# Kernel tuning notes

Hardware: AMD Instinct MI355X
Metric: run time of the kernel (lower is better)

## Reference

```python
import jax, jax.numpy as jnp
import numpy as np

E2M1_GRID = jnp.array([0.0, 0.5, 1.0, 1.5, 2.0, 3.0, 4.0, 6.0], dtype=jnp.float32)
E2M1_MIDS = (E2M1_GRID[1:] + E2M1_GRID[:-1]) / 2.0
FP4_MAX = 6.0
FP8_E4M3_MAX = 448.0


def nvfp4_quant_dequant(w):
    # Emulates tetrajetv2.quant_fp4_dequant_trans_fused: two-level scaling
    # (fp32 outer scale per 128 inputs, fp8-e4m3 inner scale per 16 inputs),
    # values rounded to the signed E2M1 grid, then dequantized.
    O, I = w.shape
    w16 = w.reshape(O, I // 128, 8, 16)
    amax128 = jnp.max(jnp.abs(w16), axis=(-2, -1))          # [O, I/128]
    outer = amax128 / (FP4_MAX * FP8_E4M3_MAX)
    outer = jnp.where(outer > 0, outer, 1.0)
    amax16 = jnp.max(jnp.abs(w16), axis=-1)                  # [O, I/128, 8]
    inner = amax16 / FP4_MAX / outer[..., None]
    inner = inner.astype(jnp.float8_e4m3fn).astype(jnp.float32)  # fp8 round
    scale = outer[..., None] * inner                          # [O, I/128, 8]
    safe = jnp.where(scale > 0, scale, 1.0)[..., None]
    code = w16 / safe
    a = jnp.abs(code)
    idx = jnp.searchsorted(E2M1_MIDS, a)                      # nearest grid pt
    q = E2M1_GRID[idx] * jnp.sign(code)
    return (q * scale[..., None]).reshape(O, I)


def setup_inputs() -> dict:
    key = jax.random.key(0)
    k0, k1, k2 = jax.random.split(key, 3)
    B, S, H = 2, 2048, 2048
    hidden_states = jax.random.normal(k0, (B, S, H), dtype=jnp.float32)
    # raw weights ~ N(0, 0.023) as in FP4Linear init, then fake-quantized
    w_qkv = jax.random.normal(k1, (3 * H, H), dtype=jnp.float32) * 0.023
    w_o = jax.random.normal(k2, (H, H), dtype=jnp.float32) * 0.023
    w_qkv = nvfp4_quant_dequant(w_qkv)
    w_o = nvfp4_quant_dequant(w_o)
    return {"hidden_states": hidden_states, "w_qkv": w_qkv, "w_o": w_o}


def reference(hidden_states, w_qkv, w_o):
    B, S, H = hidden_states.shape
    num_heads = 16
    head_dim = H // num_heads
    qkv = jnp.einsum('bsh,oh->bso', hidden_states, w_qkv)      # [B,S,3H]
    qkv = qkv.reshape(B, S, 3, num_heads, head_dim)
    qkv = jnp.transpose(qkv, (2, 0, 3, 1, 4))                  # [3,B,nh,S,hd]
    q, k, v = qkv[0], qkv[1], qkv[2]
    scale = 1.0 / jnp.sqrt(jnp.float32(head_dim))
    scores = jnp.einsum('bhqd,bhkd->bhqk', q, k) * scale
    causal = jnp.tril(jnp.ones((S, S), dtype=bool))
    scores = jnp.where(causal, scores, jnp.finfo(scores.dtype).min)
    probs = jax.nn.softmax(scores, axis=-1)
    attn = jnp.einsum('bhqk,bhkd->bhqd', probs, v)             # [B,nh,S,hd]
    attn = jnp.transpose(attn, (0, 2, 1, 3)).reshape(B, S, H)
    return jnp.einsum('bsh,oh->bso', attn, w_o)
```

## Files before the change

### kernel.cpp

```cpp
#include <hip/hip_runtime.h>
#include <hip/hip_bf16.h>
#include <stdint.h>

typedef __bf16 bf16x8 __attribute__((ext_vector_type(8)));
typedef float f32x4 __attribute__((ext_vector_type(4)));

#define AS1 __attribute__((address_space(1)))
#define AS3 __attribute__((address_space(3)))

#define PBAR() do { __builtin_amdgcn_sched_barrier(0); asm volatile("s_barrier" ::: "memory"); __builtin_amdgcn_sched_barrier(0); } while (0)
#define LGK0() do { asm volatile("s_waitcnt lgkmcnt(0)" ::: "memory"); __builtin_amdgcn_sched_barrier(0); } while (0)
#define VMCNT(n) do { asm volatile("s_waitcnt vmcnt(" #n ")" ::: "memory"); __builtin_amdgcn_sched_barrier(0); } while (0)

__device__ __forceinline__ unsigned short f2bf(float x) {
    union { float f; uint32_t u; } v; v.f = x;
    uint32_t r = v.u + 0x7fffu + ((v.u >> 16) & 1u);
    return (unsigned short)(r >> 16);
}

__global__ void k_f2bf3(const float* __restrict__ a, unsigned short* __restrict__ oa, int na4,
                        const float* __restrict__ b, unsigned short* __restrict__ ob, int nb4,
                        const float* __restrict__ c, unsigned short* __restrict__ oc, int nc4) {
    int i = blockIdx.x * blockDim.x + threadIdx.x;
    const float* src; unsigned short* dst; int j;
    if (i < na4)            { src = a; dst = oa; j = i; }
    else if (i < na4 + nb4) { src = b; dst = ob; j = i - na4; }
    else if (i < na4 + nb4 + nc4) { src = c; dst = oc; j = i - na4 - nb4; }
    else return;
    float4 v = reinterpret_cast<const float4*>(src)[j];
    ushort4 o;
    o.x = f2bf(v.x); o.y = f2bf(v.y); o.z = f2bf(v.z); o.w = f2bf(v.w);
    reinterpret_cast<ushort4*>(dst)[j] = o;
}

template <typename TOUT>
__global__ __launch_bounds__(512, 2) void k_gemm128x256(
    const unsigned short* __restrict__ A,
    const unsigned short* __restrict__ B,
    TOUT* __restrict__ C, int M, int N, int K, int ngrid)
{
    __shared__ __align__(16) unsigned short Albuf[3][4096];
    __shared__ __align__(16) unsigned short Blbuf[3][8192];
    const int tid = threadIdx.x, lane = tid & 63, wv = tid >> 6;
    const int wr = wv >> 2, wc = wv & 3;
    const int fl = lane & 15, fg = lane >> 4;
    const int cpx = ngrid >> 3;
    const int sw = ((int)blockIdx.x & 7) * cpx + ((int)blockIdx.x >> 3);
    const int bm = sw & 31, bn = sw >> 5;
    const int nK = K >> 5;

    const unsigned short* Ag = A + (size_t)bm * 128 * K;
    const unsigned short* Bg = B + (size_t)bn * 256 * K;

    auto stageA = [&](int buf, int t) {
        const int r = tid >> 2;
        const int cs = (tid & 3) ^ ((r >> 1) & 3);
        const unsigned short* src = Ag + (size_t)r * K + t * 32 + cs * 8;
        __builtin_amdgcn_global_load_lds((const AS1 void*)src,
            (AS3 void*)((char*)&Albuf[buf][0] + wv * 1024), 16, 0, 0);
    };
    auto stageB = [&](int buf, int half, int t) {
        const int r = tid >> 2;
        const int cs = (tid & 3) ^ ((r >> 1) & 3);
        const unsigned short* src = Bg + (size_t)(half * 128 + r) * K + t * 32 + cs * 8;
        __builtin_amdgcn_global_load_lds((const AS1 void*)src,
            (AS3 void*)((char*)&Blbuf[buf][0] + half * 8192 + wv * 1024), 16, 0, 0);
    };
    auto ldfrag = [&](const unsigned short* base, int r) -> bf16x8 {
        return *reinterpret_cast<const bf16x8*>(
            (const char*)base + r * 64 + ((fg ^ ((r >> 1) & 3)) << 4));
    };

    f32x4 acc[4][4];
#pragma unroll
    for (int i = 0; i < 4; ++i)
#pragma unroll
        for (int j = 0; j < 4; ++j) acc[i][j] = (f32x4){0.f, 0.f, 0.f, 0.f};

    stageA(0, 0); stageB(0, 0, 0); stageB(0, 1, 0);
    stageA(1, 1); stageB(1, 0, 1); stageB(1, 1, 1);
    asm volatile("s_waitcnt vmcnt(3)" ::: "memory");
    PBAR();

    int c = 0;
    for (int t = 0; t < nK; ++t) {
        const unsigned short* Ac = Albuf[c];
        const unsigned short* Bc = Blbuf[c];
        bf16x8 af[4], bv[4];
#pragma unroll
        for (int i = 0; i < 4; ++i) af[i] = ldfrag(Ac, wr * 64 + i * 16 + fl);
#pragma unroll
        for (int j = 0; j < 4; ++j) bv[j] = ldfrag(Bc, wc * 64 + j * 16 + fl);
        if (t + 2 < nK) {
            int nb = c + 2; if (nb >= 3) nb -= 3;
            stageA(nb, t + 2); stageB(nb, 0, t + 2); stageB(nb, 1, t + 2);
        }
        PBAR();
        LGK0();
        __builtin_amdgcn_s_setprio(1);
#pragma unroll
        for (int i = 0; i < 4; ++i)
#pragma unroll
            for (int j = 0; j < 4; ++j)
                acc[i][j] = __builtin_amdgcn_mfma_f32_16x16x32_bf16(af[i], bv[j], acc[i][j], 0, 0, 0);
        __builtin_amdgcn_s_setprio(0);
        if (t + 2 < nK)      { asm volatile("s_waitcnt vmcnt(3)" ::: "memory"); }
        else if (t + 1 < nK) { asm volatile("s_waitcnt vmcnt(0)" ::: "memory"); }
        PBAR();
        ++c; if (c == 3) c = 0;
    }

#pragma unroll
    for (int i = 0; i < 4; ++i)
#pragma unroll
        for (int j = 0; j < 4; ++j)
#pragma unroll
            for (int r = 0; r < 4; ++r) {
                int row = bm * 128 + wr * 64 + i * 16 + fg * 4 + r;
                int col = bn * 256 + wc * 64 + j * 16 + fl;
                float v = acc[i][j][r];
                if constexpr (sizeof(TOUT) == 2)
                    ((unsigned short*)C)[(size_t)row * N + col] = f2bf(v);
                else
                    C[(size_t)row * N + col] = v;
            }
}

template <typename TOUT>
__global__ __launch_bounds__(256, 3) void k_gemm128x128(
    const unsigned short* __restrict__ A,
    const unsigned short* __restrict__ B,
    TOUT* __restrict__ C, int M, int N, int K, int ngrid)
{
    __shared__ __align__(16) unsigned short Al[3][4096];
    __shared__ __align__(16) unsigned short Bl[3][4096];
    const int tid = threadIdx.x, lane = tid & 63, wv = tid >> 6;
    const int wr = wv >> 1, wc = wv & 1;
    const int fl = lane & 15, fg = lane >> 4;
    const int nbm = M >> 7;
    const int cpx = ngrid >> 3;
    const int sw = ((int)blockIdx.x & 7) * cpx + ((int)blockIdx.x >> 3);
    const int bm = sw % nbm, bn = sw / nbm;
    const int nK = K >> 5;

    const unsigned short* Ag = A + (size_t)bm * 128 * K;
    const unsigned short* Bg = B + (size_t)bn * 128 * K;

    auto stage = [&](int buf, int t) {
#pragma unroll
        for (int u = 0; u < 2; ++u) {
            int ch = u * 256 + tid;
            int r = ch >> 2, cs = (ch & 3) ^ ((r >> 1) & 3);
            __builtin_amdgcn_global_load_lds(
                (const AS1 void*)(Ag + (size_t)r * K + t * 32 + cs * 8),
                (AS3 void*)((char*)&Al[buf][0] + (u * 256 + wv * 64) * 16), 16, 0, 0);
        }
#pragma unroll
        for (int u = 0; u < 2; ++u) {
            int ch = u * 256 + tid;
            int r = ch >> 2, cs = (ch & 3) ^ ((r >> 1) & 3);
            __builtin_amdgcn_global_load_lds(
                (const AS1 void*)(Bg + (size_t)r * K + t * 32 + cs * 8),
                (AS3 void*)((char*)&Bl[buf][0] + (u * 256 + wv * 64) * 16), 16, 0, 0);
        }
    };
    auto ldfrag = [&](const unsigned short* base, int r) -> bf16x8 {
        return *reinterpret_cast<const bf16x8*>(
            (const char*)base + r * 64 + ((fg ^ ((r >> 1) & 3)) << 4));
    };

    f32x4 acc[4][4];
#pragma unroll
    for (int i = 0; i < 4; ++i)
#pragma unroll
        for (int j = 0; j < 4; ++j) acc[i][j] = (f32x4){0.f, 0.f, 0.f, 0.f};

    stage(0, 0);
    stage(1, 1);
    asm volatile("s_waitcnt vmcnt(4)" ::: "memory");
    PBAR();

    int c = 0;
    for (int t = 0; t < nK; ++t) {
        const unsigned short* Ac = Al[c];
        const unsigned short* Bc = Bl[c];
        bf16x8 af[4], bv[4];
#pragma unroll
        for (int i = 0; i < 4; ++i) af[i] = ldfrag(Ac, wr * 64 + i * 16 + fl);
#pragma unroll
        for (int j = 0; j < 4; ++j) bv[j] = ldfrag(Bc, wc * 64 + j * 16 + fl);
        if (t + 2 < nK) {
            int nb = c + 2; if (nb >= 3) nb -= 3;
            stage(nb, t + 2);
        }
        PBAR();
        LGK0();
        __builtin_amdgcn_s_setprio(1);
#pragma unroll
        for (int i = 0; i < 4; ++i)
#pragma unroll
            for (int j = 0; j < 4; ++j)
                acc[i][j] = __builtin_amdgcn_mfma_f32_16x16x32_bf16(af[i], bv[j], acc[i][j], 0, 0, 0);
        __builtin_amdgcn_s_setprio(0);
        if (t + 2 < nK)      { asm volatile("s_waitcnt vmcnt(4)" ::: "memory"); }
        else if (t + 1 < nK) { asm volatile("s_waitcnt vmcnt(0)" ::: "memory"); }
        PBAR();
        ++c; if (c == 3) c = 0;
    }

#pragma unroll
    for (int i = 0; i < 4; ++i)
#pragma unroll
        for (int j = 0; j < 4; ++j)
#pragma unroll
            for (int r = 0; r < 4; ++r) {
                int row = bm * 128 + wr * 64 + i * 16 + fg * 4 + r;
                int col = bn * 128 + wc * 64 + j * 16 + fl;
                float v = acc[i][j][r];
                if constexpr (sizeof(TOUT) == 2)
                    ((unsigned short*)C)[(size_t)row * N + col] = f2bf(v);
                else
                    C[(size_t)row * N + col] = v;
            }
}

__global__ void k_transpose_v(const unsigned short* __restrict__ qkv, unsigned short* __restrict__ vT) {
    __shared__ unsigned short t[32][33];
    const int bh = blockIdx.z;
    const int b = bh >> 4, h = bh & 15;
    const int s0 = blockIdx.x * 32, d0 = blockIdx.y * 32;
    const int tx = threadIdx.x, ty = threadIdx.y;
#pragma unroll
    for (int i = 0; i < 4; ++i) {
        int s = s0 + ty + i * 8;
        t[ty + i * 8][tx] = qkv[(size_t)(b * 2048 + s) * 6144 + 4096 + h * 128 + d0 + tx];
    }
    __syncthreads();
#pragma unroll
    for (int i = 0; i < 4; ++i) {
        int d = d0 + ty + i * 8;
        vT[((size_t)bh * 128 + d) * 2048 + s0 + tx] = t[tx][ty + i * 8];
    }
}

__global__ __launch_bounds__(256, 2) void k_attn(
    const unsigned short* __restrict__ qkv, const unsigned short* __restrict__ vT,
    unsigned short* __restrict__ out)
{
    __shared__ unsigned short Klds[2][8192];
    __shared__ unsigned short Vlds[8192];
    __shared__ __align__(16) unsigned short Plds[4][2048];

    const int tid = threadIdx.x, lane = tid & 63, wv = tid >> 6;
    const int fl = lane & 15, fg = lane >> 4;
    const int bh = blockIdx.y;
    const int qb = (bh >= 16) ? blockIdx.x : 15 - blockIdx.x;
    const int b = bh >> 4, h = bh & 15;
    const int q0w = qb * 128 + wv * 32;
    const size_t base = (size_t)b * 2048 * 6144 + (size_t)h * 128;
    const unsigned short* Qbase = qkv + base;
    const unsigned short* Kbase = qkv + base + 2048;
    const unsigned short* Vbase = vT + (size_t)bh * 128 * 2048;
    unsigned short* pw = Plds[wv];

    bf16x8 qf[2][4];
#pragma unroll
    for (int m = 0; m < 2; ++m)
#pragma unroll
        for (int kk = 0; kk < 4; ++kk)
            qf[m][kk] = *reinterpret_cast<const bf16x8*>(
                Qbase + (size_t)(q0w + m * 16 + fl) * 6144 + kk * 32 + fg * 8);
    asm volatile("s_waitcnt vmcnt(0)" ::: "memory");
    __builtin_amdgcn_sched_barrier(0);

    auto stageK = [&](int buf, int kv0) {
#pragma unroll
        for (int rnd = 0; rnd < 4; ++rnd) {
            int ch = rnd * 256 + tid;
            int row = ch >> 4;
            int cbl = ((ch & 15) << 4) ^ ((row & 7) << 4);
            const unsigned short* src = Kbase + (size_t)(kv0 + row) * 6144 + (cbl >> 1);
            __builtin_amdgcn_global_load_lds((const AS1 void*)src,
                (AS3 void*)((char*)&Klds[buf][0] + (rnd * 256 + wv * 64) * 16), 16, 0, 0);
        }
    };
    auto stageV = [&](int kv0) {
#pragma unroll
        for (int rnd = 0; rnd < 4; ++rnd) {
            int ch = rnd * 256 + tid;
            int row = ch >> 3;
            int cbl = ((ch & 7) << 4) ^ ((row & 7) << 4);
            const unsigned short* src = Vbase + (size_t)row * 2048 + kv0 + (cbl >> 1);
            __builtin_amdgcn_global_load_lds((const AS1 void*)src,
                (AS3 void*)((char*)&Vlds[0] + (rnd * 256 + wv * 64) * 16), 16, 0, 0);
        }
    };

    f32x4 acc[2][8];
#pragma unroll
    for (int m = 0; m < 2; ++m)
#pragma unroll
        for (int nb = 0; nb < 8; ++nb) acc[m][nb] = (f32x4){0.f, 0.f, 0.f, 0.f};
    float l_r[2] = {0.f, 0.f};
    const float sc2 = 0.12751879523473098f;
    const float c2  = 14.426950408889634f;
    const int nIter = 2 * qb + 2;

    stageK(0, 0);

    for (int it = 0; it < nIter; ++it) {
        const int kv0 = it * 64;
        const bool act = (kv0 <= q0w + 31);
        const bool haveK = (it + 1 < nIter);
        stageV(kv0);
        if (haveK) stageK((it + 1) & 1, kv0 + 64);
        __builtin_amdgcn_sched_barrier(0);
        if (haveK) { VMCNT(8); } else { VMCNT(4); }
        PBAR();
        if (act) {
            const bool full = (kv0 + 63 <= q0w);
            const unsigned short* Kb = Klds[it & 1];
            f32x4 s[2][4];
#pragma unroll
            for (int m = 0; m < 2; ++m)
#pragma unroll
                for (int n = 0; n < 4; ++n) s[m][n] = (f32x4){0.f, 0.f, 0.f, 0.f};
            __builtin_amdgcn_s_setprio(1);
#pragma unroll
            for (int kk = 0; kk < 4; ++kk)
#pragma unroll
                for (int n = 0; n < 4; ++n) {
                    const int row = n * 16 + fl;
                    bf16x8 kf = *reinterpret_cast<const bf16x8*>(
                        (const char*)Kb + row * 256 + ((kk * 64 + fg * 16) ^ ((row & 7) << 4)));
                    s[0][n] = __builtin_amdgcn_mfma_f32_16x16x32_bf16(kf, qf[0][kk], s[0][n], 0, 0, 0);
                    s[1][n] = __builtin_amdgcn_mfma_f32_16x16x32_bf16(kf, qf[1][kk], s[1][n], 0, 0, 0);
                }
            __builtin_amdgcn_s_setprio(0);
#pragma unroll
            for (int m = 0; m < 2; ++m) {
                const int qi = q0w + m * 16 + fl;
                const int prow = m * 16 + fl;
                const int rb = prow * 128, swz = (prow & 7) << 4;
#pragma unroll
                for (int n = 0; n < 4; ++n) {
                    const int kbase = kv0 + n * 16 + fg * 4;
                    float v0 = s[m][n][0] * sc2, v1 = s[m][n][1] * sc2,
                          v2 = s[m][n][2] * sc2, v3 = s[m][n][3] * sc2;
                    if (!full) {
                        if (kbase     > qi) v0 = -3e38f;
                        if (kbase + 1 > qi) v1 = -3e38f;
                        if (kbase + 2 > qi) v2 = -3e38f;
                        if (kbase + 3 > qi) v3 = -3e38f;
                    }
                    float p0 = __builtin_amdgcn_exp2f(v0 - c2), p1 = __builtin_amdgcn_exp2f(v1 - c2),
                          p2 = __builtin_amdgcn_exp2f(v2 - c2), p3 = __builtin_amdgcn_exp2f(v3 - c2);
                    l_r[m] += p0 + p1 + p2 + p3;
                    uint32_t lo = (uint32_t)f2bf(p0) | ((uint32_t)f2bf(p1) << 16);
                    uint32_t hi = (uint32_t)f2bf(p2) | ((uint32_t)f2bf(p3) << 16);
                    const int byte = rb + ((n * 32 + fg * 8) ^ swz);
                    uint2 pk; pk.x = lo; pk.y = hi;
                    *reinterpret_cast<uint2*>((char*)pw + byte) = pk;
                }
            }
            LGK0();
        }
        if (haveK) { VMCNT(4); } else { VMCNT(0); }
        PBAR();
        if (act) {
            bf16x8 pf[2][2];
#pragma unroll
            for (int m = 0; m < 2; ++m)
#pragma unroll
                for (int k2 = 0; k2 < 2; ++k2) {
                    const int row = m * 16 + fl;
                    pf[m][k2] = *reinterpret_cast<const bf16x8*>(
                        (const char*)pw + row * 128 + ((k2 * 64 + fg * 16) ^ ((row & 7) << 4)));
                }
            __builtin_amdgcn_s_setprio(1);
#pragma unroll
            for (int nb = 0; nb < 8; ++nb)
#pragma unroll
                for (int k2 = 0; k2 < 2; ++k2) {
                    const int d = nb * 16 + fl;
                    bf16x8 vf = *reinterpret_cast<const bf16x8*>(
                        (const char*)Vlds + d * 128 + ((k2 * 64 + fg * 16) ^ ((d & 7) << 4)));
                    acc[0][nb] = __builtin_amdgcn_mfma_f32_16x16x32_bf16(pf[0][k2], vf, acc[0][nb], 0, 0, 0);
                    acc[1][nb] = __builtin_amdgcn_mfma_f32_16x16x32_bf16(pf[1][k2], vf, acc[1][nb], 0, 0, 0);
                }
            __builtin_amdgcn_s_setprio(0);
        }
        PBAR();
    }

#pragma unroll
    for (int m = 0; m < 2; ++m) {
        float l = l_r[m];
        l += __shfl_xor(l, 16);
        l += __shfl_xor(l, 32);
        float inv[4];
#pragma unroll
        for (int r = 0; r < 4; ++r) inv[r] = 1.0f / __shfl(l, fg * 4 + r);
#pragma unroll
        for (int nb = 0; nb < 8; ++nb)
#pragma unroll
            for (int r = 0; r < 4; ++r) {
                int row = q0w + m * 16 + fg * 4 + r;
                int col = h * 128 + nb * 16 + fl;
                out[(size_t)(b * 2048 + row) * 2048 + col] = f2bf(acc[m][nb][r] * inv[r]);
            }
    }
}

extern "C" void kernel_launch(void* const* d_in, const int* in_sizes, int n_in,
                              void* d_out, int out_size, void* d_ws, size_t ws_size,
                              hipStream_t stream) {
    const float* hs   = (const float*)d_in[0];
    const float* wqkv = (const float*)d_in[1];
    const float* wo   = (const float*)d_in[2];
    float* out = (float*)d_out;

    char* p = (char*)d_ws;
    unsigned short* Xb    = (unsigned short*)p; p += (size_t)4096 * 2048 * 2;
    unsigned short* Wqkvb = (unsigned short*)p; p += (size_t)6144 * 2048 * 2;
    unsigned short* Wob   = (unsigned short*)p; p += (size_t)2048 * 2048 * 2;
    unsigned short* QKV   = (unsigned short*)p; p += (size_t)4096 * 6144 * 2;
    unsigned short* VT    = (unsigned short*)p; p += (size_t)32 * 128 * 2048 * 2;
    unsigned short* ATTN  = (unsigned short*)p; p += (size_t)4096 * 2048 * 2;

    k_f2bf3<<<24576, 256, 0, stream>>>(hs, Xb, 2097152, wqkv, Wqkvb, 3145728, wo, Wob, 1048576);
    k_gemm128x256<unsigned short><<<768, 512, 0, stream>>>(Xb, Wqkvb, QKV, 4096, 6144, 2048, 768);
    k_transpose_v<<<dim3(64, 4, 32), dim3(32, 8), 0, stream>>>(QKV, VT);
    k_attn<<<dim3(16, 32), 256, 0, stream>>>(QKV, VT, ATTN);
    k_gemm128x128<float><<<512, 256, 0, stream>>>(ATTN, Wob, out, 4096, 2048, 2048, 512);
}
```

Before: 254.0 us.

## Pair causal query tiles per attention block with 8 waves of 16 rows

The attention kernel now launches 512-thread blocks, each with 8 waves owning 16 query rows, and each block handles two query tiles (jb and 15-jb) in sequence so causal work is balanced across blocks. The grid drops from 16x32 to 8x32 blocks. Each K/V tile staged in LDS now feeds 8 waves instead of 4, and per-wave register use (accumulators, Q fragments) is halved. In exchange, each wave issues half as many MFMAs per LDS fragment read, there are fewer blocks to spread across CUs, and the two phases run serially inside a block.

```diff
diff --git a/kernel.cpp b/kernel.cpp
--- a/kernel.cpp
+++ b/kernel.cpp
@@ -243,110 +243,105 @@
     }
 }
 
-__global__ __launch_bounds__(256, 2) void k_attn(
+__global__ __launch_bounds__(512, 2) void k_attn(
     const unsigned short* __restrict__ qkv, const unsigned short* __restrict__ vT,
     unsigned short* __restrict__ out)
 {
     __shared__ unsigned short Klds[2][8192];
     __shared__ unsigned short Vlds[8192];
-    __shared__ __align__(16) unsigned short Plds[4][2048];
+    __shared__ __align__(16) unsigned short Plds[8][1024];
 
     const int tid = threadIdx.x, lane = tid & 63, wv = tid >> 6;
     const int fl = lane & 15, fg = lane >> 4;
+    const int jb = blockIdx.x;
     const int bh = blockIdx.y;
-    const int qb = (bh >= 16) ? blockIdx.x : 15 - blockIdx.x;
     const int b = bh >> 4, h = bh & 15;
-    const int q0w = qb * 128 + wv * 32;
     const size_t base = (size_t)b * 2048 * 6144 + (size_t)h * 128;
     const unsigned short* Qbase = qkv + base;
     const unsigned short* Kbase = qkv + base + 2048;
     const unsigned short* Vbase = vT + (size_t)bh * 128 * 2048;
     unsigned short* pw = Plds[wv];
 
-    bf16x8 qf[2][4];
-#pragma unroll
-    for (int m = 0; m < 2; ++m)
-#pragma unroll
-        for (int kk = 0; kk < 4; ++kk)
-            qf[m][kk] = *reinterpret_cast<const bf16x8*>(
-                Qbase + (size_t)(q0w + m * 16 + fl) * 6144 + kk * 32 + fg * 8);
-    asm volatile("s_waitcnt vmcnt(0)" ::: "memory");
-    __builtin_amdgcn_sched_barrier(0);
-
     auto stageK = [&](int buf, int kv0) {
 #pragma unroll
-        for (int rnd = 0; rnd < 4; ++rnd) {
-            int ch = rnd * 256 + tid;
+        for (int rnd = 0; rnd < 2; ++rnd) {
+            int ch = rnd * 512 + tid;
             int row = ch >> 4;
             int cbl = ((ch & 15) << 4) ^ ((row & 7) << 4);
             const unsigned short* src = Kbase + (size_t)(kv0 + row) * 6144 + (cbl >> 1);
             __builtin_amdgcn_global_load_lds((const AS1 void*)src,
-                (AS3 void*)((char*)&Klds[buf][0] + (rnd * 256 + wv * 64) * 16), 16, 0, 0);
+                (AS3 void*)((char*)&Klds[buf][0] + (rnd * 512 + wv * 64) * 16), 16, 0, 0);
         }
     };
     auto stageV = [&](int kv0) {
 #pragma unroll
-        for (int rnd = 0; rnd < 4; ++rnd) {
-            int ch = rnd * 256 + tid;
+        for (int rnd = 0; rnd < 2; ++rnd) {
+            int ch = rnd * 512 + tid;
             int row = ch >> 3;
             int cbl = ((ch & 7) << 4) ^ ((row & 7) << 4);
             const unsigned short* src = Vbase + (size_t)row * 2048 + kv0 + (cbl >> 1);
             __builtin_amdgcn_global_load_lds((const AS1 void*)src,
-                (AS3 void*)((char*)&Vlds[0] + (rnd * 256 + wv * 64) * 16), 16, 0, 0);
-        }
-    };
-
-    f32x4 acc[2][8];
-#pragma unroll
-    for (int m = 0; m < 2; ++m)
-#pragma unroll
-        for (int nb = 0; nb < 8; ++nb) acc[m][nb] = (f32x4){0.f, 0.f, 0.f, 0.f};
-    float l_r[2] = {0.f, 0.f};
+                (AS3 void*)((char*)&Vlds[0] + (rnd * 512 + wv * 64) * 16), 16, 0, 0);
+        }
+    };
+
     const float sc2 = 0.12751879523473098f;
     const float c2  = 14.426950408889634f;
-    const int nIter = 2 * qb + 2;
-
-    stageK(0, 0);
-
-    for (int it = 0; it < nIter; ++it) {
-        const int kv0 = it * 64;
-        const bool act = (kv0 <= q0w + 31);
-        const bool haveK = (it + 1 < nIter);
-        stageV(kv0);
-        if (haveK) stageK((it + 1) & 1, kv0 + 64);
+
+#pragma unroll 1
+    for (int phase = 0; phase < 2; ++phase) {
+        const int tile = phase ? (15 - jb) : jb;
+        const int q0w = tile * 128 + wv * 16;
+
+        bf16x8 qf[4];
+#pragma unroll
+        for (int kk = 0; kk < 4; ++kk)
+            qf[kk] = *reinterpret_cast<const bf16x8*>(
+                Qbase + (size_t)(q0w + fl) * 6144 + kk * 32 + fg * 8);
+        asm volatile("s_waitcnt vmcnt(0)" ::: "memory");
         __builtin_amdgcn_sched_barrier(0);
-        if (haveK) { VMCNT(8); } else { VMCNT(4); }
-        PBAR();
-        if (act) {
-            const bool full = (kv0 + 63 <= q0w);
-            const unsigned short* Kb = Klds[it & 1];
-            f32x4 s[2][4];
-#pragma unroll
-            for (int m = 0; m < 2; ++m)
-#pragma unroll
-                for (int n = 0; n < 4; ++n) s[m][n] = (f32x4){0.f, 0.f, 0.f, 0.f};
-            __builtin_amdgcn_s_setprio(1);
-#pragma unroll
-            for (int kk = 0; kk < 4; ++kk)
-#pragma unroll
-                for (int n = 0; n < 4; ++n) {
-                    const int row = n * 16 + fl;
-                    bf16x8 kf = *reinterpret_cast<const bf16x8*>(
-                        (const char*)Kb + row * 256 + ((kk * 64 + fg * 16) ^ ((row & 7) << 4)));
-                    s[0][n] = __builtin_amdgcn_mfma_f32_16x16x32_bf16(kf, qf[0][kk], s[0][n], 0, 0, 0);
-                    s[1][n] = __builtin_amdgcn_mfma_f32_16x16x32_bf16(kf, qf[1][kk], s[1][n], 0, 0, 0);
-                }
-            __builtin_amdgcn_s_setprio(0);
-#pragma unroll
-            for (int m = 0; m < 2; ++m) {
-                const int qi = q0w + m * 16 + fl;
-                const int prow = m * 16 + fl;
-                const int rb = prow * 128, swz = (prow & 7) << 4;
+
+        f32x4 acc[8];
+#pragma unroll
+        for (int nb = 0; nb < 8; ++nb) acc[nb] = (f32x4){0.f, 0.f, 0.f, 0.f};
+        float l_r = 0.f;
+        const int nIter = 2 * tile + 2;
+
+        stageK(0, 0);
+
+        for (int it = 0; it < nIter; ++it) {
+            const int kv0 = it * 64;
+            const bool act = (kv0 <= q0w + 15);
+            const bool haveK = (it + 1 < nIter);
+            stageV(kv0);
+            if (haveK) stageK((it + 1) & 1, kv0 + 64);
+            __builtin_amdgcn_sched_barrier(0);
+            if (haveK) { VMCNT(4); } else { VMCNT(2); }
+            PBAR();
+            if (act) {
+                const bool full = (kv0 + 63 <= q0w);
+                const unsigned short* Kb = Klds[it & 1];
+                f32x4 s[4];
+#pragma unroll
+                for (int n = 0; n < 4; ++n) s[n] = (f32x4){0.f, 0.f, 0.f, 0.f};
+                __builtin_amdgcn_s_setprio(1);
+#pragma unroll
+                for (int kk = 0; kk < 4; ++kk)
+#pragma unroll
+                    for (int n = 0; n < 4; ++n) {
+                        const int row = n * 16 + fl;
+                        bf16x8 kf = *reinterpret_cast<const bf16x8*>(
+                            (const char*)Kb + row * 256 + ((kk * 64 + fg * 16) ^ ((row & 7) << 4)));
+                        s[n] = __builtin_amdgcn_mfma_f32_16x16x32_bf16(kf, qf[kk], s[n], 0, 0, 0);
+                    }
+                __builtin_amdgcn_s_setprio(0);
+                const int qi = q0w + fl;
+                const int rb = fl * 128, swz = (fl & 7) << 4;
 #pragma unroll
                 for (int n = 0; n < 4; ++n) {
                     const int kbase = kv0 + n * 16 + fg * 4;
-                    float v0 = s[m][n][0] * sc2, v1 = s[m][n][1] * sc2,
-                          v2 = s[m][n][2] * sc2, v3 = s[m][n][3] * sc2;
+                    float v0 = s[n][0] * sc2, v1 = s[n][1] * sc2,
+                          v2 = s[n][2] * sc2, v3 = s[n][3] * sc2;
                     if (!full) {
                         if (kbase     > qi) v0 = -3e38f;
                         if (kbase + 1 > qi) v1 = -3e38f;
@@ -355,47 +350,39 @@
                     }
                     float p0 = __builtin_amdgcn_exp2f(v0 - c2), p1 = __builtin_amdgcn_exp2f(v1 - c2),
                           p2 = __builtin_amdgcn_exp2f(v2 - c2), p3 = __builtin_amdgcn_exp2f(v3 - c2);
-                    l_r[m] += p0 + p1 + p2 + p3;
+                    l_r += p0 + p1 + p2 + p3;
                     uint32_t lo = (uint32_t)f2bf(p0) | ((uint32_t)f2bf(p1) << 16);
                     uint32_t hi = (uint32_t)f2bf(p2) | ((uint32_t)f2bf(p3) << 16);
                     const int byte = rb + ((n * 32 + fg * 8) ^ swz);
                     uint2 pk; pk.x = lo; pk.y = hi;
                     *reinterpret_cast<uint2*>((char*)pw + byte) = pk;
                 }
+                LGK0();
             }
-            LGK0();
-        }
-        if (haveK) { VMCNT(4); } else { VMCNT(0); }
-        PBAR();
-        if (act) {
-            bf16x8 pf[2][2];
-#pragma unroll
-            for (int m = 0; m < 2; ++m)
-#pragma unroll
-                for (int k2 = 0; k2 < 2; ++k2) {
-                    const int row = m * 16 + fl;
-                    pf[m][k2] = *reinterpret_cast<const bf16x8*>(
-                        (const char*)pw + row * 128 + ((k2 * 64 + fg * 16) ^ ((row & 7) << 4)));
-                }
-            __builtin_amdgcn_s_setprio(1);
-#pragma unroll
-            for (int nb = 0; nb < 8; ++nb)
-#pragma unroll
-                for (int k2 = 0; k2 < 2; ++k2) {
-                    const int d = nb * 16 + fl;
-                    bf16x8 vf = *reinterpret_cast<const bf16x8*>(
-                        (const char*)Vlds + d * 128 + ((k2 * 64 + fg * 16) ^ ((d & 7) << 4)));
-                    acc[0][nb] = __builtin_amdgcn_mfma_f32_16x16x32_bf16(pf[0][k2], vf, acc[0][nb], 0, 0, 0);
-                    acc[1][nb] = __builtin_amdgcn_mfma_f32_16x16x32_bf16(pf[1][k2], vf, acc[1][nb], 0, 0, 0);
-                }
-            __builtin_amdgcn_s_setprio(0);
-        }
-        PBAR();
-    }
-
-#pragma unroll
-    for (int m = 0; m < 2; ++m) {
-        float l = l_r[m];
+            if (haveK) { VMCNT(2); } else { VMCNT(0); }
+            PBAR();
+            if (act) {
+                bf16x8 pf[2];
+#pragma unroll
+                for (int k2 = 0; k2 < 2; ++k2)
+                    pf[k2] = *reinterpret_cast<const bf16x8*>(
+                        (const char*)pw + fl * 128 + ((k2 * 64 + fg * 16) ^ ((fl & 7) << 4)));
+                __builtin_amdgcn_s_setprio(1);
+#pragma unroll
+                for (int nb = 0; nb < 8; ++nb)
+#pragma unroll
+                    for (int k2 = 0; k2 < 2; ++k2) {
+                        const int d = nb * 16 + fl;
+                        bf16x8 vf = *reinterpret_cast<const bf16x8*>(
+                            (const char*)Vlds + d * 128 + ((k2 * 64 + fg * 16) ^ ((d & 7) << 4)));
+                        acc[nb] = __builtin_amdgcn_mfma_f32_16x16x32_bf16(pf[k2], vf, acc[nb], 0, 0, 0);
+                    }
+                __builtin_amdgcn_s_setprio(0);
+            }
+            PBAR();
+        }
+
+        float l = l_r;
         l += __shfl_xor(l, 16);
         l += __shfl_xor(l, 32);
         float inv[4];
@@ -405,9 +392,9 @@
         for (int nb = 0; nb < 8; ++nb)
 #pragma unroll
             for (int r = 0; r < 4; ++r) {
-                int row = q0w + m * 16 + fg * 4 + r;
+                int row = q0w + fg * 4 + r;
                 int col = h * 128 + nb * 16 + fl;
-                out[(size_t)(b * 2048 + row) * 2048 + col] = f2bf(acc[m][nb][r] * inv[r]);
+                out[(size_t)(b * 2048 + row) * 2048 + col] = f2bf(acc[nb][r] * inv[r]);
             }
     }
 }
@@ -431,6 +418,6 @@
     k_f2bf3<<<24576, 256, 0, stream>>>(hs, Xb, 2097152, wqkv, Wqkvb, 3145728, wo, Wob, 1048576);
     k_gemm128x256<unsigned short><<<768, 512, 0, stream>>>(Xb, Wqkvb, QKV, 4096, 6144, 2048, 768);
     k_transpose_v<<<dim3(64, 4, 32), dim3(32, 8), 0, stream>>>(QKV, VT);
-    k_attn<<<dim3(16, 32), 256, 0, stream>>>(QKV, VT, ATTN);
+    k_attn<<<dim3(8, 32), 512, 0, stream>>>(QKV, VT, ATTN);
     k_gemm128x128<float><<<512, 256, 0, stream>>>(ATTN, Wob, out, 4096, 2048, 2048, 512);
 }
```

New measurement: 260.3 us. +2.5%, slower.
